# Performance work log

Hardware: AMD Instinct MI355X
Metric: run time of the kernel (lower is better)

## Reference

```python
import jax, jax.numpy as jnp
import numpy as np

EMBED_SIZE = 768
HEAD_SIZE = 64
B, T = 4, 2048


def setup_inputs() -> dict:
    key = jax.random.key(0)
    kx, kk, kq, kv = jax.random.split(key, 4)
    x = jax.random.normal(kx, (B, T, EMBED_SIZE), dtype=jnp.float32)
    # torch Linear(E, H, bias=False): weight [H, E]; stored here as [E, H] for x @ W
    s = 1.0 / np.sqrt(EMBED_SIZE)
    Wk = jax.random.uniform(kk, (EMBED_SIZE, HEAD_SIZE), jnp.float32, -s, s)
    Wq = jax.random.uniform(kq, (EMBED_SIZE, HEAD_SIZE), jnp.float32, -s, s)
    Wv = jax.random.uniform(kv, (EMBED_SIZE, HEAD_SIZE), jnp.float32, -s, s)
    return {"x": x, "Wk": Wk, "Wq": Wq, "Wv": Wv}


def reference(x, Wk, Wq, Wv):
    Bx, Tx, E = x.shape
    k = x @ Wk  # [B, T, H]
    q = x @ Wq
    v = x @ Wv
    w = jnp.einsum("bth,bsh->bts", q, k)  # [B, T, T]
    causal = jnp.tril(jnp.ones((Tx, Tx), dtype=bool))
    # Faithful to source: mask to -inf FIRST, then scale by sqrt(embed_size)
    w = jnp.where(causal, w, -jnp.inf)
    w = w / jnp.sqrt(jnp.asarray(E, dtype=x.dtype))
    w = jax.nn.softmax(w, axis=-1)
    # dropout: eval mode / identity for the correctness baseline
    return jnp.einsum("bts,bsh->bth", w, v)
```

## Files before the change

kernel.cpp:

```cpp
#include <hip/hip_runtime.h>
#include <hip/hip_bf16.h>


typedef __attribute__((ext_vector_type(8))) short short8;
typedef __attribute__((ext_vector_type(4))) float f32x4;

#define SPLIT_KB 4
#define MAX_SP 8

__device__ __forceinline__ unsigned short f2bf(float f) {
    union { float f; unsigned u; } v; v.f = f;
    unsigned r = v.u + 0x7fffu + ((v.u >> 16) & 1u);
    return (unsigned short)(r >> 16);
}

__global__ __launch_bounds__(256) void proj_kernel(const float* __restrict__ x,
                                                   const float* __restrict__ Wk,
                                                   const float* __restrict__ Wq,
                                                   const float* __restrict__ Wv,
                                                   unsigned short* __restrict__ qws,
                                                   unsigned short* __restrict__ kws,
                                                   unsigned short* __restrict__ vT) {
    __shared__ unsigned short xs[32 * 72];
    __shared__ unsigned short wsm[64 * 72];
    const float CSCALE = 1.4426950408889634f / 27.712812921102035f;
    int tid = threadIdx.x;
    int lane = tid & 63, wave = tid >> 6;
    int quad = lane >> 4, l16 = lane & 15;
    int row0 = blockIdx.x * 32;
    int my = blockIdx.y;
    const float* W = (my == 0) ? Wq : (my == 1) ? Wk : Wv;

    int xrow = tid >> 3, xcb = (tid & 7) * 8;
    int wn = tid & 63, wk0 = (tid >> 6) * 16;

    f32x4 acc[2];
    acc[0] = (f32x4)(0.f); acc[1] = (f32x4)(0.f);

    for (int kc = 0; kc < 12; ++kc) {
        __syncthreads();
        {
            const float* src = x + (size_t)(row0 + xrow) * 768 + kc * 64 + xcb;
            float4 f0 = *(const float4*)(src);
            float4 f1 = *(const float4*)(src + 4);
            short8 pk;
            pk[0] = (short)f2bf(f0.x); pk[1] = (short)f2bf(f0.y);
            pk[2] = (short)f2bf(f0.z); pk[3] = (short)f2bf(f0.w);
            pk[4] = (short)f2bf(f1.x); pk[5] = (short)f2bf(f1.y);
            pk[6] = (short)f2bf(f1.z); pk[7] = (short)f2bf(f1.w);
            *(short8*)&xs[xrow * 72 + xcb] = pk;
        }
        {
            float wv[16];
            for (int i = 0; i < 16; ++i)
                wv[i] = W[(size_t)(kc * 64 + wk0 + i) * 64 + wn];
            if (my == 0)
                for (int i = 0; i < 16; ++i) wv[i] *= CSCALE;
            short8 p0, p1;
            for (int i = 0; i < 8; ++i) { p0[i] = (short)f2bf(wv[i]); p1[i] = (short)f2bf(wv[8 + i]); }
            *(short8*)&wsm[wn * 72 + wk0] = p0;
            *(short8*)&wsm[wn * 72 + wk0 + 8] = p1;
        }
        __syncthreads();
        for (int kh = 0; kh < 2; ++kh) {
            int kk = kh * 32 + quad * 8;
            short8 bfr = *(const short8*)&wsm[(wave * 16 + l16) * 72 + kk];
            for (int mt = 0; mt < 2; ++mt) {
                short8 a = *(const short8*)&xs[(mt * 16 + l16) * 72 + kk];
                acc[mt] = __builtin_amdgcn_mfma_f32_16x16x32_bf16(a, bfr, acc[mt], 0, 0, 0);
            }
        }
    }
    __syncthreads();
    int n = wave * 16 + l16;
    if (my != 2) {
        unsigned short* dst = (my == 0) ? qws : kws;
        for (int mt = 0; mt < 2; ++mt)
            for (int j = 0; j < 4; ++j) {
                int rloc = mt * 16 + quad * 4 + j;
                dst[(size_t)(row0 + rloc) * 64 + n] = f2bf(acc[mt][j]);
            }
    } else {
        for (int mt = 0; mt < 2; ++mt)
            for (int j = 0; j < 4; ++j) {
                int rloc = mt * 16 + quad * 4 + j;
                wsm[n * 40 + rloc] = f2bf(acc[mt][j]);
            }
        __syncthreads();
        int bidx = row0 >> 11, t0 = row0 & 2047;
        int c = tid >> 2, rb = (tid & 3) * 8;
        *(short8*)&vT[((size_t)(bidx * 64 + c)) * 2048 + t0 + rb] =
            *(const short8*)&wsm[c * 40 + rb];
    }
}

__global__ __launch_bounds__(128) void attn_split(const unsigned short* __restrict__ qws,
                                                  const unsigned short* __restrict__ kws,
                                                  const unsigned short* __restrict__ vT,
                                                  float* __restrict__ po,
                                                  float* __restrict__ pl,
                                                  float* __restrict__ out) {
    int bx = blockIdx.x, b = blockIdx.y, sp = blockIdx.z;
    int kbmax = (bx >> 1) + 1;
    int nsp = (kbmax + SPLIT_KB - 1) / SPLIT_KB;
    if (sp >= nsp) return;
    int kb_lo = sp * SPLIT_KB;
    int kb_hi = min(kb_lo + SPLIT_KB, kbmax);

    __shared__ unsigned short qs[32 * 72];
    __shared__ unsigned short ks[64 * 72];
    __shared__ unsigned short vs[64 * 72];
    __shared__ unsigned short ps[2][16 * 72];
    int tid = threadIdx.x;
    int lane = tid & 63, wave = tid >> 6;
    int quad = lane >> 4, l16 = lane & 15;
    int q0 = bx * 32;
    size_t qbase = ((size_t)b * 2048 + q0) * 64;
    for (int i = 0; i < 2; ++i) {
        int e = tid + 128 * i;
        int r = e >> 3, hb = (e & 7) * 8;
        *(short8*)&qs[r * 72 + hb] = *(const short8*)&qws[qbase + r * 64 + hb];
    }
    __syncthreads();
    short8 aq[2];
    for (int kh = 0; kh < 2; ++kh)
        aq[kh] = *(const short8*)&qs[(wave * 16 + l16) * 72 + kh * 32 + quad * 8];

    f32x4 o_acc[4];
    for (int nt = 0; nt < 4; ++nt) o_acc[nt] = (f32x4)(0.f);
    float l_run[4];
    int row_g[4];
    for (int j = 0; j < 4; ++j) {
        l_run[j] = 0.f;
        row_g[j] = q0 + wave * 16 + quad * 4 + j;
    }

    for (int kb = kb_lo; kb < kb_hi; ++kb) {
        __syncthreads();
        size_t kvbase = ((size_t)b * 2048 + kb * 64) * 64;
        for (int i = 0; i < 4; ++i) {
            int e = tid + 128 * i;
            int r = e >> 3, hb = (e & 7) * 8;
            *(short8*)&ks[r * 72 + hb] = *(const short8*)&kws[kvbase + r * 64 + hb];
        }
        for (int i = 0; i < 4; ++i) {
            int e = tid + 128 * i;
            int h = e >> 3, kyb = (e & 7) * 8;
            *(short8*)&vs[h * 72 + kyb] =
                *(const short8*)&vT[((size_t)b * 64 + h) * 2048 + kb * 64 + kyb];
        }
        __syncthreads();
        f32x4 s[4];
        for (int nt = 0; nt < 4; ++nt) s[nt] = (f32x4)(0.f);
        for (int kh = 0; kh < 2; ++kh)
            for (int nt = 0; nt < 4; ++nt) {
                short8 bk = *(const short8*)&ks[(nt * 16 + l16) * 72 + kh * 32 + quad * 8];
                s[nt] = __builtin_amdgcn_mfma_f32_16x16x32_bf16(aq[kh], bk, s[nt], 0, 0, 0);
            }
        if (kb == kbmax - 1) {
            for (int nt = 0; nt < 4; ++nt) {
                int key = kb * 64 + nt * 16 + l16;
                for (int j = 0; j < 4; ++j)
                    if (key > row_g[j]) s[nt][j] = -1e30f;
            }
        }
        for (int nt = 0; nt < 4; ++nt)
            for (int j = 0; j < 4; ++j) {
                float p = exp2f(s[nt][j]);
                l_run[j] += p;
                ps[wave][(quad * 4 + j) * 72 + nt * 16 + l16] = f2bf(p);
            }
        for (int kh = 0; kh < 2; ++kh) {
            short8 ap = *(const short8*)&ps[wave][l16 * 72 + kh * 32 + quad * 8];
            for (int nt = 0; nt < 4; ++nt) {
                short8 bv = *(const short8*)&vs[(nt * 16 + l16) * 72 + kh * 32 + quad * 8];
                o_acc[nt] = __builtin_amdgcn_mfma_f32_16x16x32_bf16(ap, bv, o_acc[nt], 0, 0, 0);
            }
        }
    }
    for (int off = 1; off < 16; off <<= 1)
        for (int j = 0; j < 4; ++j)
            l_run[j] += __shfl_xor(l_run[j], off, 16);

    if (nsp == 1) {
        for (int nt = 0; nt < 4; ++nt)
            for (int j = 0; j < 4; ++j)
                out[((size_t)b * 2048 + row_g[j]) * 64 + nt * 16 + l16] =
                    o_acc[nt][j] / l_run[j];
        return;
    }
    int sbase = ((b * 64 + bx) * MAX_SP + sp) * 32;
    for (int nt = 0; nt < 4; ++nt)
        for (int j = 0; j < 4; ++j) {
            int r = wave * 16 + quad * 4 + j;
            po[(size_t)(sbase + r) * 64 + nt * 16 + l16] = o_acc[nt][j];
        }
    if (l16 == 0) {
        for (int j = 0; j < 4; ++j) {
            int r = wave * 16 + quad * 4 + j;
            pl[sbase + r] = l_run[j];
        }
    }
}

__global__ __launch_bounds__(256) void reduce_kernel(const float* __restrict__ po,
                                                     const float* __restrict__ pl,
                                                     float* __restrict__ out) {
    int tid = threadIdx.x;
    int lane = tid & 63, wave = tid >> 6;
    int g = blockIdx.x * 4 + wave;
    int b = g >> 11, t = g & 2047;
    int bx = t >> 5, r = t & 31;
    int kbmax = (bx >> 1) + 1;
    int nsp = (kbmax + SPLIT_KB - 1) / SPLIT_KB;
    if (nsp == 1) return;
    int base = ((b * 64 + bx) * MAX_SP) * 32 + r;
    float acc = 0.f, lsum = 0.f;
    for (int sp = 0; sp < nsp; ++sp) {
        acc += po[(size_t)(base + sp * 32) * 64 + lane];
        lsum += pl[base + sp * 32];
    }
    out[(size_t)g * 64 + lane] = acc / lsum;
}

extern "C" void kernel_launch(void* const* d_in, const int* in_sizes, int n_in,
                              void* d_out, int out_size, void* d_ws, size_t ws_size,
                              hipStream_t stream) {
    const float* x  = (const float*)d_in[0];
    const float* Wk = (const float*)d_in[1];
    const float* Wq = (const float*)d_in[2];
    const float* Wv = (const float*)d_in[3];
    float* out = (float*)d_out;
    char* w = (char*)d_ws;
    unsigned short* qws = (unsigned short*)w;
    unsigned short* kws = (unsigned short*)(w + 1048576);
    unsigned short* vT  = (unsigned short*)(w + 2097152);
    float* po = (float*)(w + 3145728);
    float* pl = (float*)(w + 19922944);
    proj_kernel<<<dim3(256, 3), 256, 0, stream>>>(x, Wk, Wq, Wv, qws, kws, vT);
    attn_split<<<dim3(64, 4, MAX_SP), 128, 0, stream>>>(qws, kws, vT, po, pl, out);
    reduce_kernel<<<2048, 256, 0, stream>>>(po, pl, out);
}
```

Before: 104.1 us.

## Load Q/K/V MFMA operands directly from global memory, bypassing shared-memory staging

The attention kernel no longer stages Q, K and V tiles through LDS. Each lane reads its MFMA fragments straight from global memory (through L1/L2), which removes two block barriers per key block and the LDS write/read round trip. The transposed V buffer gets a padded leading dimension (2080) to avoid cache-set conflicts on strided reads, and the workspace offsets move to fit it. The risk is that waves now issue more redundant global loads with higher latency and no cooperative reuse across waves.

New measurement: 108.3 us. 1.04x slower.

```diff
diff --git a/kernel.cpp b/kernel.cpp
--- a/kernel.cpp
+++ b/kernel.cpp
@@ -7,6 +7,7 @@
 
 #define SPLIT_KB 4
 #define MAX_SP 8
+#define VT_LD 2080
 
 __device__ __forceinline__ unsigned short f2bf(float f) {
     union { float f; unsigned u; } v; v.f = f;
@@ -89,7 +90,7 @@
         __syncthreads();
         int bidx = row0 >> 11, t0 = row0 & 2047;
         int c = tid >> 2, rb = (tid & 3) * 8;
-        *(short8*)&vT[((size_t)(bidx * 64 + c)) * 2048 + t0 + rb] =
+        *(short8*)&vT[((size_t)(bidx * 64 + c)) * VT_LD + t0 + rb] =
             *(const short8*)&wsm[c * 40 + rb];
     }
 }
@@ -107,24 +108,18 @@
     int kb_lo = sp * SPLIT_KB;
     int kb_hi = min(kb_lo + SPLIT_KB, kbmax);
 
-    __shared__ unsigned short qs[32 * 72];
-    __shared__ unsigned short ks[64 * 72];
-    __shared__ unsigned short vs[64 * 72];
     __shared__ unsigned short ps[2][16 * 72];
     int tid = threadIdx.x;
     int lane = tid & 63, wave = tid >> 6;
     int quad = lane >> 4, l16 = lane & 15;
     int q0 = bx * 32;
-    size_t qbase = ((size_t)b * 2048 + q0) * 64;
-    for (int i = 0; i < 2; ++i) {
-        int e = tid + 128 * i;
-        int r = e >> 3, hb = (e & 7) * 8;
-        *(short8*)&qs[r * 72 + hb] = *(const short8*)&qws[qbase + r * 64 + hb];
-    }
-    __syncthreads();
+
     short8 aq[2];
-    for (int kh = 0; kh < 2; ++kh)
-        aq[kh] = *(const short8*)&qs[(wave * 16 + l16) * 72 + kh * 32 + quad * 8];
+    {
+        const unsigned short* qp = qws + ((size_t)b * 2048 + q0 + wave * 16 + l16) * 64;
+        aq[0] = *(const short8*)(qp + quad * 8);
+        aq[1] = *(const short8*)(qp + 32 + quad * 8);
+    }
 
     f32x4 o_acc[4];
     for (int nt = 0; nt < 4; ++nt) o_acc[nt] = (f32x4)(0.f);
@@ -136,25 +131,12 @@
     }
 
     for (int kb = kb_lo; kb < kb_hi; ++kb) {
-        __syncthreads();
-        size_t kvbase = ((size_t)b * 2048 + kb * 64) * 64;
-        for (int i = 0; i < 4; ++i) {
-            int e = tid + 128 * i;
-            int r = e >> 3, hb = (e & 7) * 8;
-            *(short8*)&ks[r * 72 + hb] = *(const short8*)&kws[kvbase + r * 64 + hb];
-        }
-        for (int i = 0; i < 4; ++i) {
-            int e = tid + 128 * i;
-            int h = e >> 3, kyb = (e & 7) * 8;
-            *(short8*)&vs[h * 72 + kyb] =
-                *(const short8*)&vT[((size_t)b * 64 + h) * 2048 + kb * 64 + kyb];
-        }
-        __syncthreads();
+        const unsigned short* kp = kws + ((size_t)b * 2048 + kb * 64) * 64;
         f32x4 s[4];
         for (int nt = 0; nt < 4; ++nt) s[nt] = (f32x4)(0.f);
         for (int kh = 0; kh < 2; ++kh)
             for (int nt = 0; nt < 4; ++nt) {
-                short8 bk = *(const short8*)&ks[(nt * 16 + l16) * 72 + kh * 32 + quad * 8];
+                short8 bk = *(const short8*)(kp + (nt * 16 + l16) * 64 + kh * 32 + quad * 8);
                 s[nt] = __builtin_amdgcn_mfma_f32_16x16x32_bf16(aq[kh], bk, s[nt], 0, 0, 0);
             }
         if (kb == kbmax - 1) {
@@ -170,10 +152,11 @@
                 l_run[j] += p;
                 ps[wave][(quad * 4 + j) * 72 + nt * 16 + l16] = f2bf(p);
             }
+        const unsigned short* vp = vT + (size_t)(b * 64) * VT_LD + kb * 64;
         for (int kh = 0; kh < 2; ++kh) {
             short8 ap = *(const short8*)&ps[wave][l16 * 72 + kh * 32 + quad * 8];
             for (int nt = 0; nt < 4; ++nt) {
-                short8 bv = *(const short8*)&vs[(nt * 16 + l16) * 72 + kh * 32 + quad * 8];
+                short8 bv = *(const short8*)(vp + (size_t)(nt * 16 + l16) * VT_LD + kh * 32 + quad * 8);
                 o_acc[nt] = __builtin_amdgcn_mfma_f32_16x16x32_bf16(ap, bv, o_acc[nt], 0, 0, 0);
             }
         }
@@ -235,8 +218,8 @@
     unsigned short* qws = (unsigned short*)w;
     unsigned short* kws = (unsigned short*)(w + 1048576);
     unsigned short* vT  = (unsigned short*)(w + 2097152);
-    float* po = (float*)(w + 3145728);
-    float* pl = (float*)(w + 19922944);
+    float* po = (float*)(w + 4194304);
+    float* pl = (float*)(w + 20971520);
     proj_kernel<<<dim3(256, 3), 256, 0, stream>>>(x, Wk, Wq, Wv, qws, kws, vT);
     attn_split<<<dim3(64, 4, MAX_SP), 128, 0, stream>>>(qws, kws, vT, po, pl, out);
     reduce_kernel<<<2048, 256, 0, stream>>>(po, pl, out);
```
